# Kernel optimization log

Measured on AMD Instinct MI355X. Metric: run time of the kernel, lower is better.

## Reference

```python
import jax, jax.numpy as jnp
from jax import lax
import numpy as np

# ---- init hyperparameters (from init_kwargs) ----
STRIDE = 1
DP_CHANNELS = 1
ATOM_R = 8
ATOM_C = 8
NUMB_ATOM = 128
T_SC = 3
K = 256
BATCH = 32
IMG = 64


def setup_inputs() -> dict:
    key = jax.random.key(0)
    k1, k2 = jax.random.split(key)
    Y = jax.random.normal(k1, (BATCH, DP_CHANNELS, IMG, IMG), dtype=jnp.float32)
    # ConvTranspose2d weight layout: (numb_atom, dp_channels, atom_c, atom_r)
    W = jax.random.normal(k2, (NUMB_ATOM, DP_CHANNELS, ATOM_C, ATOM_R), dtype=jnp.float32)
    # normalise_weights(): each (i, j) filter divided by its L2 norm
    W = W / jnp.sqrt(jnp.sum(W ** 2, axis=(2, 3), keepdims=True))
    return {"Y": Y, "W_D": W}


def _conv_D(X, W):
    # PyTorch ConvTranspose2d (stride=1, no padding): full convolution with
    # spatially-flipped kernel; W is (in=numb_atom, out=dp_channels, kh, kw).
    kh, kw = W.shape[2], W.shape[3]
    return lax.conv_general_dilated(
        X, jnp.flip(W, (2, 3)), (1, 1),
        [(kh - 1, kh - 1), (kw - 1, kw - 1)],
        dimension_numbers=('NCHW', 'IOHW', 'NCHW'))


def _conv_Dt(R, Wt):
    # PyTorch Conv2d (VALID, stride=1): Wt is (out=numb_atom, in=dp, kh, kw)
    return lax.conv_general_dilated(
        R, Wt, (1, 1), 'VALID', dimension_numbers=('NCHW', 'OIHW', 'NCHW'))


def _hard_threshold_k(X, k):
    # keep the k largest-|.| entries per sample (over flattened C,H,W)
    B = X.shape[0]
    flat = X.reshape(B, -1)
    _, idx = lax.top_k(jnp.abs(flat), k)                      # [B, k]
    vals = jnp.take_along_axis(flat, idx, axis=1)             # [B, k]
    out = jnp.zeros_like(flat).at[jnp.arange(B)[:, None], idx].set(vals)
    return out.reshape(X.shape)


def _linesearch(Y, X, W, Wt, k):
    R = Y - _conv_D(X, W)
    g = _conv_Dt(R, Wt)
    l2_start = jnp.sum(R ** 2)

    def attempt(alpha):
        Xu = _hard_threshold_k(X + alpha * g, k)
        err = jnp.sum((Y - _conv_D(Xu, W)) ** 2)
        return Xu, err

    Xu0, err0 = attempt(jnp.float32(1.0))

    def cond(s):
        _, _, err, count = s
        return (err >= l2_start) & (count <= 15)

    def body(s):
        alpha, _, _, count = s
        alpha = alpha * jnp.float32(0.5)
        Xu, err = attempt(alpha)
        return (alpha, Xu, err, count + 1)

    alpha, Xu, err, _ = lax.while_loop(
        cond, body, (jnp.float32(1.0), Xu0, err0, jnp.int32(0)))
    return Xu, err, alpha


def reference(Y, W_D):
    # D_trans.weight = D.weight.permute(0,1,3,2) -> (numb_atom, dp, atom_r, atom_c)
    Wt = jnp.swapaxes(W_D, 2, 3)
    kh, kw = Wt.shape[2], Wt.shape[3]
    B, _, H, W_sp = Y.shape
    X = jnp.zeros((B, W_D.shape[0], H - kh + 1, W_sp - kw + 1), dtype=Y.dtype)
    for _ in range(T_SC):
        X, _, _ = _linesearch(Y, X, W_D, Wt, K)
    return X
```

## Files before the change

### kernel.cpp

```cpp
#include <hip/hip_runtime.h>
#include <stdint.h>

#define NB   32
#define NCH  128
#define IMG  64
#define IMG2 4096
#define OH   57
#define OHW  3249
#define CHW  415872
#define KTOP 256
#define NATT 17
#define NS   32
#define SCAP 512
#define CAP2 8192
#define NCAP 2048
#define NREG 8
#define NBUCK 8192
#define HSHIFT 18
#define TGT  512
#define RSTRIDE 72

__global__ void k_init(int* support_cnt) {
    if (threadIdx.x < NB) support_cnt[threadIdx.x] = 0;
}

__global__ void k_zero(uint32_t* hist, int* cand_cnt) {
    int i = blockIdx.x * 256 + threadIdx.x;
    if (i < NB * NBUCK) hist[i] = 0;
    if (i < NB * NS) cand_cnt[i] = 0;
}

__global__ __launch_bounds__(256) void k_resid(
    const float* __restrict__ Y, const float* __restrict__ W,
    const int* __restrict__ support_cnt, const uint32_t* __restrict__ support_idx,
    const float* __restrict__ support_val, float* __restrict__ Rg, double* __restrict__ l2part)
{
    int b = blockIdx.x, tid = threadIdx.x;
    __shared__ float Rs[IMG2];
    const float4* Y4 = (const float4*)(Y + b * IMG2);
    float4* R4 = (float4*)Rs;
    for (int i = tid; i < IMG2 / 4; i += 256) R4[i] = Y4[i];
    __syncthreads();
    int n = support_cnt[b];
    for (int task = tid; task < n * 64; task += 256) {
        int i = task >> 6, tap = task & 63, p = tap >> 3, q = tap & 7;
        uint32_t idx = support_idx[b * KTOP + i];
        float val = support_val[b * KTOP + i];
        int c = idx / OHW, rem = idx % OHW, s = rem / OH, t = rem % OH;
        float w = W[c * 64 + p * 8 + q];
        atomicAdd(&Rs[(s + p) * IMG + (t + q)], -val * w);
    }
    __syncthreads();
    double acc = 0.0;
    for (int i = tid; i < IMG2; i += 256) {
        float v = Rs[i];
        Rg[b * IMG2 + i] = v;
        acc += (double)v * (double)v;
    }
    __shared__ double red[256];
    red[tid] = acc; __syncthreads();
    for (int s2 = 128; s2 > 0; s2 >>= 1) { if (tid < s2) red[tid] += red[tid + s2]; __syncthreads(); }
    if (tid == 0) l2part[b] = red[0];
}

__global__ __launch_bounds__(256) void k_conv(
    const float* __restrict__ Rg, const float* __restrict__ W,
    float* __restrict__ g_out, uint32_t* __restrict__ hist)
{
    int b = blockIdx.x, cg0 = blockIdx.y, tid = threadIdx.x;
    __shared__ float Rs[71 * 72];
    __shared__ uint32_t hl[NBUCK];
    for (int i = tid; i < 71 * 72; i += 256) Rs[i] = 0.f;
    for (int i = tid; i < NBUCK; i += 256) hl[i] = 0u;
    __syncthreads();
    const float4* R4 = (const float4*)(Rg + b * IMG2);
    for (int i = tid; i < 1024; i += 256) {
        int row = i >> 4, col4 = (i & 15) * 4;
        *(float4*)&Rs[row * 72 + col4] = R4[i];
    }
    __syncthreads();
    int csub = tid >> 7;
    int tile = tid & 127;
    bool active = tile < 120;
    int tr = active ? tile / 15 : 0;
    int tc = active ? tile % 15 : 0;
    int s0 = tr * 8, t0 = tc * 4;

    for (int sub = 0; sub < 4; ++sub) {
        int c = cg0 * 8 + sub * 2 + csub;
        int c_s = __builtin_amdgcn_readfirstlane(c);
        const float* Wc = W + c_s * 64;

        float acc[8][4];
#pragma unroll
        for (int r = 0; r < 8; ++r)
#pragma unroll
            for (int cc = 0; cc < 4; ++cc) acc[r][cc] = 0.f;

#pragma unroll
        for (int rho = 0; rho < 15; ++rho) {
            float rb[12];
            const float* rp = &Rs[(s0 + rho) * 72 + t0];
            *(float4*)&rb[0] = *(const float4*)rp;
            *(float4*)&rb[4] = *(const float4*)(rp + 4);
            *(float4*)&rb[8] = *(const float4*)(rp + 8);
#pragma unroll
            for (int r = 0; r < 8; ++r) {
                const int p = rho - r;
                if (p >= 0 && p < 8) {
#pragma unroll
                    for (int q = 0; q < 8; ++q) {
                        float wv = Wc[q * 8 + p];
#pragma unroll
                        for (int cc = 0; cc < 4; ++cc)
                            acc[r][cc] = fmaf(rb[cc + q], wv, acc[r][cc]);
                    }
                }
            }
        }
        if (active) {
            float* go = g_out + (size_t)(b * NCH + c) * OHW;
#pragma unroll
            for (int r = 0; r < 8; ++r) {
                int s = s0 + r;
                if (s < OH) {
#pragma unroll
                    for (int cc = 0; cc < 4; ++cc) {
                        int t = t0 + cc;
                        if (t < OH) {
                            float v = acc[r][cc];
                            go[s * OH + t] = v;
                            uint32_t bits = __float_as_uint(v) & 0x7fffffffu;
                            atomicAdd(&hl[bits >> HSHIFT], 1u);
                        }
                    }
                }
            }
        }
    }
    __syncthreads();
    for (int i = tid; i < NBUCK; i += 256) {
        uint32_t v = hl[i];
        if (v) atomicAdd(&hist[b * NBUCK + i], v);
    }
}

__global__ __launch_bounds__(256) void k_thresh(const uint32_t* __restrict__ hist,
                                                uint32_t* __restrict__ thr) {
    int b = blockIdx.x, tid = threadIdx.x;
    uint32_t h[32];
    uint32_t s = 0;
    const uint32_t* hb = hist + b * NBUCK + tid * 32;
#pragma unroll
    for (int k = 0; k < 32; ++k) { h[k] = hb[k]; s += h[k]; }
    __shared__ uint32_t buf[2][256];
    int cur = 0;
    buf[0][tid] = s;
    __syncthreads();
    for (int d = 1; d < 256; d <<= 1) {
        uint32_t v = buf[cur][tid];
        if (tid + d < 256) v += buf[cur][tid + d];
        buf[cur ^ 1][tid] = v;
        cur ^= 1;
        __syncthreads();
    }
    uint32_t sufme = buf[cur][tid];
    uint32_t base  = (tid < 255) ? buf[cur][tid + 1] : 0u;
    if (tid == 0 && buf[cur][0] < TGT) thr[b] = 0u;
    if (base < TGT && sufme >= TGT) {
        uint32_t acc = base; int bk = 0;
#pragma unroll
        for (int k = 31; k >= 0; --k) {
            acc += h[k];
            if (acc >= TGT) { bk = tid * 32 + k; break; }
        }
        thr[b] = (uint32_t)bk << HSHIFT;
    }
}

__global__ __launch_bounds__(256) void k_collect(
    const float* __restrict__ g, const uint32_t* __restrict__ thr,
    int* __restrict__ cand_cnt, uint32_t* __restrict__ cand_idx, float* __restrict__ cand_g)
{
    int b = blockIdx.y;
    int i4 = blockIdx.x * 256 + threadIdx.x;
    if (i4 >= CHW / 4) return;
    int slice = blockIdx.x & (NS - 1);
    uint32_t tb = thr[b];
    float4 v4 = ((const float4*)(g + (size_t)b * CHW))[i4];
    float vv[4] = { v4.x, v4.y, v4.z, v4.w };
#pragma unroll
    for (int k = 0; k < 4; ++k) {
        uint32_t bits = __float_as_uint(vv[k]) & 0x7fffffffu;
        if (bits >= tb) {
            int pos = atomicAdd(&cand_cnt[b * NS + slice], 1);
            if (pos < SCAP) {
                cand_idx[(b * NS + slice) * SCAP + pos] = (uint32_t)(i4 * 4 + k);
                cand_g[(b * NS + slice) * SCAP + pos] = vv[k];
            }
        }
    }
}

__global__ __launch_bounds__(256) void k_suppg(
    const float* __restrict__ g, const uint32_t* __restrict__ thr,
    const int* __restrict__ support_cnt, const uint32_t* __restrict__ support_idx,
    const float* __restrict__ support_val,
    const int* __restrict__ cand_cnt, const uint32_t* __restrict__ cand_idx,
    const float* __restrict__ cand_g,
    uint32_t* __restrict__ c2_idx, float* __restrict__ c2_g, float* __restrict__ c2_x,
    int* __restrict__ nc_out)
{
    int b = blockIdx.x, tid = threadIdx.x;
    __shared__ uint32_t sidx[KTOP];
    __shared__ float sval[KTOP];
    __shared__ int cnts[NS];
    __shared__ int soff[NS + 1];
    __shared__ int extra;
    int n = support_cnt[b];
    if (tid < NS) cnts[tid] = min(cand_cnt[b * NS + tid], SCAP);
    if (tid == 0) extra = 0;
    if (tid < n) { sidx[tid] = support_idx[b * KTOP + tid]; sval[tid] = support_val[b * KTOP + tid]; }
    __syncthreads();
    if (tid < n) {
        uint32_t idx = sidx[tid];
        float gv = g[(size_t)b * CHW + idx];
        uint32_t bits = __float_as_uint(gv) & 0x7fffffffu;
        if (bits < thr[b]) {
            int p = atomicAdd(&extra, 1);
            c2_idx[b * CAP2 + p] = idx; c2_g[b * CAP2 + p] = gv;
        }
    }
    __syncthreads();
    __shared__ int nc_sh;
    if (tid == 0) {
        int acc = extra;
        for (int s = 0; s < NS; ++s) { soff[s] = acc; acc += cnts[s]; }
        soff[NS] = acc;
        nc_sh = min(acc, NCAP);
        nc_out[b] = nc_sh;
    }
    __syncthreads();
    for (int t = tid; t < NS * SCAP; t += 256) {
        int s = t >> 9, j = t & (SCAP - 1);
        if (j < cnts[s]) {
            int d = soff[s] + j;
            if (d < NCAP) {
                c2_idx[b * CAP2 + d] = cand_idx[(b * NS + s) * SCAP + j];
                c2_g[b * CAP2 + d] = cand_g[(b * NS + s) * SCAP + j];
            }
        }
    }
    __syncthreads();
    int nc = nc_sh;
    for (int j = tid; j < nc; j += 256) {
        uint32_t q = c2_idx[b * CAP2 + j];
        float x = 0.f;
        int lo = 0, hi = n - 1;
        while (lo <= hi) {
            int mid = (lo + hi) >> 1;
            uint32_t m = sidx[mid];
            if (m == q) { x = sval[mid]; break; }
            if (m < q) lo = mid + 1; else hi = mid - 1;
        }
        c2_x[b * CAP2 + j] = x;
    }
}

__global__ __launch_bounds__(256) void k_attempt(
    const float* __restrict__ Y, const float* __restrict__ W,
    const int* __restrict__ nc_in, const uint32_t* __restrict__ cand_idx,
    const float* __restrict__ cand_g, const float* __restrict__ cand_x,
    uint32_t* __restrict__ sel_idx, float* __restrict__ sel_val, double* __restrict__ err)
{
    int a = blockIdx.x, b = blockIdx.y, tid = threadIdx.x;
    int lane = tid & 63, wid = tid >> 6;
    float alpha = ldexpf(1.f, -a);
    int nc = min(nc_in[b], NCAP);
    const uint32_t* ci = cand_idx + b * CAP2;
    const float* cgp = cand_g + b * CAP2;
    const float* cxp = cand_x + b * CAP2;

    __shared__ int wcnt[2][4];
    __shared__ int nsel_sh, ntie_sh;
    __shared__ uint32_t s_cidx[KTOP];
    __shared__ float s_v[KTOP];
    __shared__ uint32_t tie_f[256];
    __shared__ float tie_v[256];
    __shared__ float recon[64 * RSTRIDE];
    __shared__ double red[256];

    float v[NREG]; uint32_t fi[NREG]; uint32_t kr[NREG];
#pragma unroll
    for (int j = 0; j < NREG; ++j) {
        int i = tid + 256 * j;
        bool ok = i < nc;
        float gg = ok ? cgp[i] : 0.f;
        float xx = ok ? cxp[i] : 0.f;
        fi[j] = ok ? ci[i] : 0xffffffffu;
        float vv = fmaf(alpha, gg, xx);
        v[j] = ok ? vv : 0.f;
        kr[j] = ok ? (__float_as_uint(vv) & 0x7fffffffu) : 0u;
    }
    if (tid == 0) { nsel_sh = 0; ntie_sh = 0; }
    s_cidx[tid] = 0u; s_v[tid] = 0.f;

    uint32_t T = 0;
    for (int bit = 30; bit >= 0; --bit) {
        uint32_t tt = T | (1u << bit);
        int lc = 0;
#pragma unroll
        for (int j = 0; j < NREG; ++j) lc += (kr[j] >= tt) ? 1 : 0;
        for (int d = 32; d > 0; d >>= 1) lc += __shfl_xor(lc, d, 64);
        if (lane == 0) wcnt[bit & 1][wid] = lc;
        __syncthreads();
        int tot = wcnt[bit & 1][0] + wcnt[bit & 1][1] + wcnt[bit & 1][2] + wcnt[bit & 1][3];
        if (tot >= KTOP) T = tt;
    }

#pragma unroll
    for (int j = 0; j < NREG; ++j) {
        bool isg = (fi[j] != 0xffffffffu) && (kr[j] > T);
        unsigned long long m = __ballot(isg);
        if (m) {
            int base = 0;
            if (lane == 0) base = atomicAdd(&nsel_sh, __popcll(m));
            base = __shfl(base, 0, 64);
            if (isg) {
                int p = base + __popcll(m & ((1ull << lane) - 1ull));
                if (p < KTOP) { s_cidx[p] = fi[j]; s_v[p] = v[j]; }
            }
        }
        bool ist = (fi[j] != 0xffffffffu) && (kr[j] == T);
        unsigned long long m2 = __ballot(ist);
        if (m2) {
            int base2 = 0;
            if (lane == 0) base2 = atomicAdd(&ntie_sh, __popcll(m2));
            base2 = __shfl(base2, 0, 64);
            if (ist) {
                int p = base2 + __popcll(m2 & ((1ull << lane) - 1ull));
                if (p < 256) { tie_f[p] = fi[j]; tie_v[p] = v[j]; }
            }
        }
    }
    __syncthreads();
    int nsel = min(nsel_sh, KTOP);
    int rem = KTOP - nsel;
    int nt = min(ntie_sh, 256);
    for (int j = tid; j < nt; j += 256) {
        uint32_t me = tie_f[j];
        int rank = 0;
        for (int j2 = 0; j2 < nt; ++j2) rank += (tie_f[j2] < me) ? 1 : 0;
        if (rank < rem) { s_cidx[nsel + rank] = me; s_v[nsel + rank] = tie_v[j]; }
    }
    __syncthreads();
    sel_idx[((size_t)a * NB + b) * KTOP + tid] = s_cidx[tid];
    sel_val[((size_t)a * NB + b) * KTOP + tid] = s_v[tid];

    for (int i = tid; i < 64 * RSTRIDE; i += 256) recon[i] = 0.f;
    __syncthreads();
    for (int task = tid; task < KTOP * 64; task += 256) {
        int i = task >> 6, tap = task & 63, p = tap >> 3, q = tap & 7;
        uint32_t idx = s_cidx[i];
        float val = s_v[i];
        int c = idx / OHW, remn = idx % OHW, s = remn / OH, t = remn % OH;
        atomicAdd(&recon[(s + p) * RSTRIDE + (t + q)], val * W[c * 64 + p * 8 + q]);
    }
    __syncthreads();
    double accd = 0.0;
    for (int e = tid; e < IMG2; e += 256) {
        float d = Y[b * IMG2 + e] - recon[(e >> 6) * RSTRIDE + (e & 63)];
        accd += (double)d * (double)d;
    }
    red[tid] = accd; __syncthreads();
    for (int s2 = 128; s2 > 0; s2 >>= 1) { if (tid < s2) red[tid] += red[tid + s2]; __syncthreads(); }
    if (tid == 0) err[a * NB + b] = red[0];
}

__global__ void k_select(const double* __restrict__ l2part, const double* __restrict__ err,
                         int* __restrict__ sel_a) {
    int tid = threadIdx.x;
    __shared__ double esum[NATT + 1];
    if (tid < NATT) {
        double e = 0.0;
        for (int b2 = 0; b2 < NB; ++b2) e += err[tid * NB + b2];
        esum[tid] = e;
    } else if (tid == NATT) {
        double l2 = 0.0;
        for (int b2 = 0; b2 < NB; ++b2) l2 += l2part[b2];
        esum[NATT] = l2;
    }
    __syncthreads();
    if (tid == 0) {
        double l2 = esum[NATT];
        int sel = NATT - 1;
        for (int a2 = 0; a2 < NATT; ++a2) if (esum[a2] < l2) { sel = a2; break; }
        *sel_a = sel;
    }
}

__global__ __launch_bounds__(256) void k_update(
    const int* __restrict__ sel_a, const uint32_t* __restrict__ sel_idx, const float* __restrict__ sel_val,
    int* __restrict__ support_cnt, uint32_t* __restrict__ support_idx, float* __restrict__ support_val)
{
    int b = blockIdx.x, tid = threadIdx.x;
    int a = *sel_a;
    __shared__ uint32_t ki[KTOP];
    __shared__ float kv[KTOP];
    ki[tid] = sel_idx[((size_t)a * NB + b) * KTOP + tid];
    kv[tid] = sel_val[((size_t)a * NB + b) * KTOP + tid];
    for (int k = 2; k <= KTOP; k <<= 1) {
        for (int j = k >> 1; j > 0; j >>= 1) {
            __syncthreads();
            int ixj = tid ^ j;
            if (ixj > tid) {
                uint32_t a0 = ki[tid], a1 = ki[ixj];
                float v0 = kv[tid], v1 = kv[ixj];
                bool up = ((tid & k) == 0);
                bool sw = up ? (a0 > a1) : (a0 < a1);
                if (sw) { ki[tid] = a1; ki[ixj] = a0; kv[tid] = v1; kv[ixj] = v0; }
            }
        }
    }
    __syncthreads();
    support_idx[b * KTOP + tid] = ki[tid];
    support_val[b * KTOP + tid] = kv[tid];
    if (tid == 0) support_cnt[b] = KTOP;
}

__global__ void k_outzero(float4* __restrict__ out) {
    int i = blockIdx.x * 256 + threadIdx.x;
    if (i < (NB * CHW) / 4) out[i] = make_float4(0.f, 0.f, 0.f, 0.f);
}

__global__ void k_scatter(const uint32_t* __restrict__ support_idx, const float* __restrict__ support_val,
                          float* __restrict__ out) {
    int b = blockIdx.x, tid = threadIdx.x;
    if (tid < KTOP) out[(size_t)b * CHW + support_idx[b * KTOP + tid]] = support_val[b * KTOP + tid];
}

static size_t align256(size_t x) { return (x + 255) & ~(size_t)255; }

extern "C" void kernel_launch(void* const* d_in, const int* in_sizes, int n_in,
                              void* d_out, int out_size, void* d_ws, size_t ws_size,
                              hipStream_t stream)
{
    const float* Y = (const float*)d_in[0];
    const float* W = (const float*)d_in[1];
    float* out = (float*)d_out;

    char* p = (char*)d_ws;
    size_t off = 0;
    auto carve = [&](size_t bytes) { void* r = p + off; off = align256(off + bytes); return r; };
    float*    Rg          = (float*)   carve(NB * IMG2 * sizeof(float));
    uint32_t* hist        = (uint32_t*)carve((size_t)NB * NBUCK * sizeof(uint32_t));
    uint32_t* thr         = (uint32_t*)carve(NB * sizeof(uint32_t));
    int*      cand_cnt    = (int*)     carve(NB * NS * sizeof(int));
    double*   l2part      = (double*)  carve(NB * sizeof(double));
    double*   err         = (double*)  carve(NATT * NB * sizeof(double));
    int*      sel_a       = (int*)     carve(sizeof(int));
    int*      support_cnt = (int*)     carve(NB * sizeof(int));
    uint32_t* support_idx = (uint32_t*)carve(NB * KTOP * sizeof(uint32_t));
    float*    support_val = (float*)   carve(NB * KTOP * sizeof(float));
    uint32_t* sel_idx     = (uint32_t*)carve((size_t)NATT * NB * KTOP * sizeof(uint32_t));
    float*    sel_val     = (float*)   carve((size_t)NATT * NB * KTOP * sizeof(float));
    uint32_t* cand_idx    = (uint32_t*)carve((size_t)NB * NS * SCAP * sizeof(uint32_t));
    float*    cand_g      = (float*)   carve((size_t)NB * NS * SCAP * sizeof(float));
    uint32_t* c2_idx      = (uint32_t*)carve((size_t)NB * CAP2 * sizeof(uint32_t));
    float*    c2_g        = (float*)   carve((size_t)NB * CAP2 * sizeof(float));
    float*    c2_x        = (float*)   carve((size_t)NB * CAP2 * sizeof(float));
    int*      nc_out      = (int*)     carve(NB * sizeof(int));
    (void)ws_size; (void)in_sizes; (void)n_in; (void)out_size;

    k_init<<<1, 64, 0, stream>>>(support_cnt);
    for (int t = 0; t < 3; ++t) {
        k_zero<<<(NB * NBUCK + 255) / 256, 256, 0, stream>>>(hist, cand_cnt);
        k_resid<<<NB, 256, 0, stream>>>(Y, W, support_cnt, support_idx, support_val, Rg, l2part);
        k_conv<<<dim3(NB, 16), 256, 0, stream>>>(Rg, W, out, hist);
        k_thresh<<<NB, 256, 0, stream>>>(hist, thr);
        k_collect<<<dim3((CHW / 4 + 255) / 256, NB), 256, 0, stream>>>(out, thr, cand_cnt, cand_idx, cand_g);
        k_suppg<<<NB, 256, 0, stream>>>(out, thr, support_cnt, support_idx, support_val,
                                        cand_cnt, cand_idx, cand_g, c2_idx, c2_g, c2_x, nc_out);
        k_attempt<<<dim3(NATT, NB), 256, 0, stream>>>(Y, W, nc_out, c2_idx, c2_g, c2_x,
                                                      sel_idx, sel_val, err);
        k_select<<<1, 64, 0, stream>>>(l2part, err, sel_a);
        k_update<<<NB, 256, 0, stream>>>(sel_a, sel_idx, sel_val, support_cnt, support_idx, support_val);
    }
    k_outzero<<<((NB * CHW) / 4 + 255) / 256, 256, 0, stream>>>((float4*)out);
    k_scatter<<<NB, 256, 0, stream>>>(support_idx, support_val, out);
}
```

Measured before the change: 694.6 us.

## Fuse zeroing and selection kernels, make attempt top-k single-wave without barriers

Folds the histogram and candidate-count zeroing into extra blocks of the residual kernel, and merges the alpha-selection kernel into the update kernel, cutting two launches per iteration. The attempt kernel's radix threshold search now runs redundantly in each wave with no block barriers per bit. Compaction is done by a single wave while the others zero the reconstruction buffer, and the bitonic sort in update becomes a rank-by-count sort. The trade-off is more register pressure (32 keys per lane), repeated work across waves, and serialized compaction in one wave.

```diff
diff --git a/kernel.cpp b/kernel.cpp
--- a/kernel.cpp
+++ b/kernel.cpp
@@ -14,28 +14,33 @@
 #define SCAP 512
 #define CAP2 8192
 #define NCAP 2048
-#define NREG 8
 #define NBUCK 8192
 #define HSHIFT 18
 #define TGT  512
 #define RSTRIDE 72
+#define NZB  257
 
 __global__ void k_init(int* support_cnt) {
     if (threadIdx.x < NB) support_cnt[threadIdx.x] = 0;
-}
-
-__global__ void k_zero(uint32_t* hist, int* cand_cnt) {
-    int i = blockIdx.x * 256 + threadIdx.x;
-    if (i < NB * NBUCK) hist[i] = 0;
-    if (i < NB * NS) cand_cnt[i] = 0;
 }
 
 __global__ __launch_bounds__(256) void k_resid(
     const float* __restrict__ Y, const float* __restrict__ W,
     const int* __restrict__ support_cnt, const uint32_t* __restrict__ support_idx,
-    const float* __restrict__ support_val, float* __restrict__ Rg, double* __restrict__ l2part)
-{
-    int b = blockIdx.x, tid = threadIdx.x;
+    const float* __restrict__ support_val, float* __restrict__ Rg, double* __restrict__ l2part,
+    uint32_t* __restrict__ hist, int* __restrict__ cand_cnt)
+{
+    int bx = blockIdx.x, tid = threadIdx.x;
+    if (bx >= NB) {
+        int zb = bx - NB;
+        if (zb < 256) {
+            ((uint4*)hist)[zb * 256 + tid] = make_uint4(0u, 0u, 0u, 0u);
+        } else {
+            ((uint4*)cand_cnt)[tid] = make_uint4(0u, 0u, 0u, 0u);
+        }
+        return;
+    }
+    int b = bx;
     __shared__ float Rs[IMG2];
     const float4* Y4 = (const float4*)(Y + b * IMG2);
     float4* R4 = (float4*)Rs;
@@ -281,84 +286,80 @@
     const float* cgp = cand_g + b * CAP2;
     const float* cxp = cand_x + b * CAP2;
 
-    __shared__ int wcnt[2][4];
-    __shared__ int nsel_sh, ntie_sh;
     __shared__ uint32_t s_cidx[KTOP];
     __shared__ float s_v[KTOP];
     __shared__ uint32_t tie_f[256];
     __shared__ float tie_v[256];
     __shared__ float recon[64 * RSTRIDE];
-    __shared__ double red[256];
-
-    float v[NREG]; uint32_t fi[NREG]; uint32_t kr[NREG];
-#pragma unroll
-    for (int j = 0; j < NREG; ++j) {
-        int i = tid + 256 * j;
+    __shared__ double redd[4];
+
+    uint32_t kr[32];
+#pragma unroll
+    for (int j = 0; j < 32; ++j) {
+        int i = lane + 64 * j;
         bool ok = i < nc;
         float gg = ok ? cgp[i] : 0.f;
         float xx = ok ? cxp[i] : 0.f;
-        fi[j] = ok ? ci[i] : 0xffffffffu;
         float vv = fmaf(alpha, gg, xx);
-        v[j] = ok ? vv : 0.f;
         kr[j] = ok ? (__float_as_uint(vv) & 0x7fffffffu) : 0u;
     }
-    if (tid == 0) { nsel_sh = 0; ntie_sh = 0; }
-    s_cidx[tid] = 0u; s_v[tid] = 0.f;
 
     uint32_t T = 0;
     for (int bit = 30; bit >= 0; --bit) {
         uint32_t tt = T | (1u << bit);
         int lc = 0;
 #pragma unroll
-        for (int j = 0; j < NREG; ++j) lc += (kr[j] >= tt) ? 1 : 0;
+        for (int j = 0; j < 32; ++j) lc += (kr[j] >= tt) ? 1 : 0;
         for (int d = 32; d > 0; d >>= 1) lc += __shfl_xor(lc, d, 64);
-        if (lane == 0) wcnt[bit & 1][wid] = lc;
-        __syncthreads();
-        int tot = wcnt[bit & 1][0] + wcnt[bit & 1][1] + wcnt[bit & 1][2] + wcnt[bit & 1][3];
-        if (tot >= KTOP) T = tt;
-    }
-
-#pragma unroll
-    for (int j = 0; j < NREG; ++j) {
-        bool isg = (fi[j] != 0xffffffffu) && (kr[j] > T);
-        unsigned long long m = __ballot(isg);
-        if (m) {
-            int base = 0;
-            if (lane == 0) base = atomicAdd(&nsel_sh, __popcll(m));
-            base = __shfl(base, 0, 64);
-            if (isg) {
-                int p = base + __popcll(m & ((1ull << lane) - 1ull));
-                if (p < KTOP) { s_cidx[p] = fi[j]; s_v[p] = v[j]; }
+        if (lc >= KTOP) T = tt;
+    }
+
+    if (wid != 0) {
+        for (int i = tid - 64; i < 64 * RSTRIDE; i += 192) recon[i] = 0.f;
+    } else {
+        unsigned long long ltm = (1ull << lane) - 1ull;
+        int base = 0, tbase = 0;
+#pragma unroll
+        for (int j = 0; j < 32; ++j) {
+            int i = lane + 64 * j;
+            bool valid = i < nc;
+            bool isg = valid && (kr[j] > T);
+            bool ist = valid && (kr[j] == T);
+            unsigned long long mg = __ballot(isg);
+            unsigned long long mt = __ballot(ist);
+            if (mg | mt) {
+                uint32_t cid = 0; float vv = 0.f;
+                if (isg || ist) {
+                    cid = ci[i];
+                    vv = fmaf(alpha, cgp[i], cxp[i]);
+                }
+                if (isg) {
+                    int p = base + __popcll(mg & ltm);
+                    if (p < KTOP) { s_cidx[p] = cid; s_v[p] = vv; }
+                }
+                if (ist) {
+                    int p = tbase + __popcll(mt & ltm);
+                    if (p < 256) { tie_f[p] = cid; tie_v[p] = vv; }
+                }
             }
-        }
-        bool ist = (fi[j] != 0xffffffffu) && (kr[j] == T);
-        unsigned long long m2 = __ballot(ist);
-        if (m2) {
-            int base2 = 0;
-            if (lane == 0) base2 = atomicAdd(&ntie_sh, __popcll(m2));
-            base2 = __shfl(base2, 0, 64);
-            if (ist) {
-                int p = base2 + __popcll(m2 & ((1ull << lane) - 1ull));
-                if (p < 256) { tie_f[p] = fi[j]; tie_v[p] = v[j]; }
-            }
-        }
-    }
-    __syncthreads();
-    int nsel = min(nsel_sh, KTOP);
-    int rem = KTOP - nsel;
-    int nt = min(ntie_sh, 256);
-    for (int j = tid; j < nt; j += 256) {
-        uint32_t me = tie_f[j];
-        int rank = 0;
-        for (int j2 = 0; j2 < nt; ++j2) rank += (tie_f[j2] < me) ? 1 : 0;
-        if (rank < rem) { s_cidx[nsel + rank] = me; s_v[nsel + rank] = tie_v[j]; }
-    }
-    __syncthreads();
+            base += __popcll(mg);
+            tbase += __popcll(mt);
+        }
+        int nsel = min(base, KTOP);
+        int rem = KTOP - nsel;
+        int nt = min(tbase, 256);
+        for (int j0 = lane; j0 < nt; j0 += 64) {
+            uint32_t me = tie_f[j0];
+            int rank = 0;
+            for (int j2 = 0; j2 < nt; ++j2) rank += (tie_f[j2] < me) ? 1 : 0;
+            if (rank < rem) { s_cidx[nsel + rank] = me; s_v[nsel + rank] = tie_v[j0]; }
+        }
+    }
+    __syncthreads();
+
     sel_idx[((size_t)a * NB + b) * KTOP + tid] = s_cidx[tid];
     sel_val[((size_t)a * NB + b) * KTOP + tid] = s_v[tid];
 
-    for (int i = tid; i < 64 * RSTRIDE; i += 256) recon[i] = 0.f;
-    __syncthreads();
     for (int task = tid; task < KTOP * 64; task += 256) {
         int i = task >> 6, tap = task & 63, p = tap >> 3, q = tap & 7;
         uint32_t idx = s_cidx[i];
@@ -367,20 +368,26 @@
         atomicAdd(&recon[(s + p) * RSTRIDE + (t + q)], val * W[c * 64 + p * 8 + q]);
     }
     __syncthreads();
+
     double accd = 0.0;
     for (int e = tid; e < IMG2; e += 256) {
         float d = Y[b * IMG2 + e] - recon[(e >> 6) * RSTRIDE + (e & 63)];
         accd += (double)d * (double)d;
     }
-    red[tid] = accd; __syncthreads();
-    for (int s2 = 128; s2 > 0; s2 >>= 1) { if (tid < s2) red[tid] += red[tid + s2]; __syncthreads(); }
-    if (tid == 0) err[a * NB + b] = red[0];
-}
-
-__global__ void k_select(const double* __restrict__ l2part, const double* __restrict__ err,
-                         int* __restrict__ sel_a) {
-    int tid = threadIdx.x;
+    for (int d = 32; d > 0; d >>= 1) accd += __shfl_xor(accd, d, 64);
+    if (lane == 0) redd[wid] = accd;
+    __syncthreads();
+    if (tid == 0) err[a * NB + b] = ((redd[0] + redd[1]) + redd[2]) + redd[3];
+}
+
+__global__ __launch_bounds__(256) void k_update(
+    const double* __restrict__ l2part, const double* __restrict__ err,
+    const uint32_t* __restrict__ sel_idx, const float* __restrict__ sel_val,
+    int* __restrict__ support_cnt, uint32_t* __restrict__ support_idx, float* __restrict__ support_val)
+{
+    int b = blockIdx.x, tid = threadIdx.x;
     __shared__ double esum[NATT + 1];
+    __shared__ int sel_sh;
     if (tid < NATT) {
         double e = 0.0;
         for (int b2 = 0; b2 < NB; ++b2) e += err[tid * NB + b2];
@@ -395,36 +402,20 @@
         double l2 = esum[NATT];
         int sel = NATT - 1;
         for (int a2 = 0; a2 < NATT; ++a2) if (esum[a2] < l2) { sel = a2; break; }
-        *sel_a = sel;
-    }
-}
-
-__global__ __launch_bounds__(256) void k_update(
-    const int* __restrict__ sel_a, const uint32_t* __restrict__ sel_idx, const float* __restrict__ sel_val,
-    int* __restrict__ support_cnt, uint32_t* __restrict__ support_idx, float* __restrict__ support_val)
-{
-    int b = blockIdx.x, tid = threadIdx.x;
-    int a = *sel_a;
+        sel_sh = sel;
+    }
+    __syncthreads();
+    int a = sel_sh;
     __shared__ uint32_t ki[KTOP];
     __shared__ float kv[KTOP];
     ki[tid] = sel_idx[((size_t)a * NB + b) * KTOP + tid];
     kv[tid] = sel_val[((size_t)a * NB + b) * KTOP + tid];
-    for (int k = 2; k <= KTOP; k <<= 1) {
-        for (int j = k >> 1; j > 0; j >>= 1) {
-            __syncthreads();
-            int ixj = tid ^ j;
-            if (ixj > tid) {
-                uint32_t a0 = ki[tid], a1 = ki[ixj];
-                float v0 = kv[tid], v1 = kv[ixj];
-                bool up = ((tid & k) == 0);
-                bool sw = up ? (a0 > a1) : (a0 < a1);
-                if (sw) { ki[tid] = a1; ki[ixj] = a0; kv[tid] = v1; kv[ixj] = v0; }
-            }
-        }
-    }
-    __syncthreads();
-    support_idx[b * KTOP + tid] = ki[tid];
-    support_val[b * KTOP + tid] = kv[tid];
+    __syncthreads();
+    uint32_t me = ki[tid];
+    int rank = 0;
+    for (int j = 0; j < KTOP; ++j) rank += (ki[j] < me) ? 1 : 0;
+    support_idx[b * KTOP + rank] = me;
+    support_val[b * KTOP + rank] = kv[tid];
     if (tid == 0) support_cnt[b] = KTOP;
 }
 
@@ -458,7 +449,6 @@
     int*      cand_cnt    = (int*)     carve(NB * NS * sizeof(int));
     double*   l2part      = (double*)  carve(NB * sizeof(double));
     double*   err         = (double*)  carve(NATT * NB * sizeof(double));
-    int*      sel_a       = (int*)     carve(sizeof(int));
     int*      support_cnt = (int*)     carve(NB * sizeof(int));
     uint32_t* support_idx = (uint32_t*)carve(NB * KTOP * sizeof(uint32_t));
     float*    support_val = (float*)   carve(NB * KTOP * sizeof(float));
@@ -474,8 +464,8 @@
 
     k_init<<<1, 64, 0, stream>>>(support_cnt);
     for (int t = 0; t < 3; ++t) {
-        k_zero<<<(NB * NBUCK + 255) / 256, 256, 0, stream>>>(hist, cand_cnt);
-        k_resid<<<NB, 256, 0, stream>>>(Y, W, support_cnt, support_idx, support_val, Rg, l2part);
+        k_resid<<<NB + NZB, 256, 0, stream>>>(Y, W, support_cnt, support_idx, support_val,
+                                              Rg, l2part, hist, cand_cnt);
         k_conv<<<dim3(NB, 16), 256, 0, stream>>>(Rg, W, out, hist);
         k_thresh<<<NB, 256, 0, stream>>>(hist, thr);
         k_collect<<<dim3((CHW / 4 + 255) / 256, NB), 256, 0, stream>>>(out, thr, cand_cnt, cand_idx, cand_g);
@@ -483,8 +473,8 @@
                                         cand_cnt, cand_idx, cand_g, c2_idx, c2_g, c2_x, nc_out);
         k_attempt<<<dim3(NATT, NB), 256, 0, stream>>>(Y, W, nc_out, c2_idx, c2_g, c2_x,
                                                       sel_idx, sel_val, err);
-        k_select<<<1, 64, 0, stream>>>(l2part, err, sel_a);
-        k_update<<<NB, 256, 0, stream>>>(sel_a, sel_idx, sel_val, support_cnt, support_idx, support_val);
+        k_update<<<NB, 256, 0, stream>>>(l2part, err, sel_idx, sel_val,
+                                         support_cnt, support_idx, support_val);
     }
     k_outzero<<<((NB * CHW) / 4 + 255) / 256, 256, 0, stream>>>((float4*)out);
     k_scatter<<<NB, 256, 0, stream>>>(support_idx, support_val, out);
```

Result: no change. 695.9 us (+0.2%).
